# Optimization experiments

Measured on AMD Instinct MI355X. Metric: run time of the kernel, lower is better.

The kernel has to match this reference:

```python
import jax, jax.numpy as jnp
import numpy as np

B, Q, N, D = 16, 64, 16384, 128


def setup_inputs() -> dict:
    key = jax.random.key(0)
    k1, k2, k3 = jax.random.split(key, 3)
    query_vector = jax.random.normal(k1, (B, Q, D), dtype=jnp.float32)
    m_A = jax.random.normal(k2, (B, N, D), dtype=jnp.float32)
    # valid node counts per batch element, in [N//2, N] so masks are non-degenerate
    node_nums = jax.random.randint(k3, (B,), N // 2, N + 1, dtype=jnp.int32)
    return {"query_vector": query_vector, "m_A": m_A, "node_nums": node_nums}


def reference(query_vector, m_A, node_nums):
    # GraphPF.forward with num_supporting_node = -1 (default path).
    # prob_logits: [B, Q, N]
    prob_logits = jnp.einsum("bqd,bnd->bqn", query_vector, m_A)
    neg = jnp.finfo(prob_logits.dtype).min
    # get_attention_mask: additive mask, 0 for valid nodes, finfo.min for padding
    valid = jnp.arange(m_A.shape[1])[None, :] < node_nums[:, None]  # [B, N]
    attention_mask = jnp.where(valid, 0.0, neg).astype(prob_logits.dtype)[:, None, :]
    masked_logits = prob_logits + attention_mask
    prob_soft = jax.nn.softmax(masked_logits, axis=-1)
    res_vector = jnp.einsum("bqn,bnd->bqd", prob_soft, m_A)
    return (res_vector, prob_soft, prob_logits)
```

## Files before the change

kernel.cpp:

```cpp
#include <hip/hip_runtime.h>
#include <math.h>

#define Bn 16
#define Qn 64
#define Nn 16384
#define Dn 128
#define NT 128
#define NTILES (Nn / NT)
#define NCHUNK 512
#define NCHUNKS (Nn / NCHUNK)

#define RES_ELEMS  (Bn * Qn * Dn)
#define SOFT_OFF   (RES_ELEMS)
#define LOG_OFF    (RES_ELEMS + Bn * Qn * Nn)

#define NEGF (-3.4e38f)

typedef __attribute__((ext_vector_type(8))) short short8;
typedef float f32x4 __attribute__((ext_vector_type(4)));

typedef union { unsigned int u[4]; short8 v; } pk8;

__device__ __forceinline__ unsigned short f2bf(float x) {
    unsigned int u = __float_as_uint(x);
    return (unsigned short)((u + 0x7FFF + ((u >> 16) & 1)) >> 16);
}
__device__ __forceinline__ float bf2f(unsigned short h) {
    return __uint_as_float(((unsigned int)h) << 16);
}

__global__ __launch_bounds__(256) void k_logits(
    const float* __restrict__ qv, const float* __restrict__ A,
    const int* __restrict__ nodeNum,
    float* __restrict__ logits,
    float* __restrict__ pmax, float* __restrict__ psum)
{
    const int b = blockIdx.y, tile = blockIdx.x;
    const int n0 = tile * NT;
    const int tid = threadIdx.x;
    const int lane = tid & 63, wave = tid >> 6;
    const int qd = lane >> 4, cc = lane & 15;

    __shared__ __align__(16) unsigned char smem[55296];
    unsigned short* QHI = (unsigned short*)smem;
    unsigned short* QLO = QHI + 64 * 72;
    unsigned short* AHI = QLO + 64 * 72;
    unsigned short* ALO = AHI + 128 * 72;
    float* CB   = (float*)smem;
    float* REDM = ((float*)smem) + 64 * 132;
    float* REDS = REDM + 64 * 17;

    f32x4 acc[4][2];
#pragma unroll
    for (int mi = 0; mi < 4; mi++)
#pragma unroll
        for (int ni = 0; ni < 2; ni++) acc[mi][ni] = 0.f;

    const float* qb = qv + (size_t)b * Qn * Dn;
    const float* Ab = A  + (size_t)b * Nn * Dn + (size_t)n0 * Dn;

    for (int kk = 0; kk < Dn; kk += 64) {
        __syncthreads();
#pragma unroll
        for (int t = 0; t < 4; t++) {
            int u = tid + t * 256;
            int row = u >> 4, c4 = u & 15;
            float4 v = *(const float4*)(qb + row * Dn + kk + c4 * 4);
            ushort4 hi, lo;
            hi.x = f2bf(v.x); lo.x = f2bf(v.x - bf2f(hi.x));
            hi.y = f2bf(v.y); lo.y = f2bf(v.y - bf2f(hi.y));
            hi.z = f2bf(v.z); lo.z = f2bf(v.z - bf2f(hi.z));
            hi.w = f2bf(v.w); lo.w = f2bf(v.w - bf2f(hi.w));
            *(ushort4*)(QHI + row * 72 + c4 * 4) = hi;
            *(ushort4*)(QLO + row * 72 + c4 * 4) = lo;
        }
#pragma unroll
        for (int t = 0; t < 8; t++) {
            int u = tid + t * 256;
            int row = u >> 4, c4 = u & 15;
            float4 v = *(const float4*)(Ab + row * Dn + kk + c4 * 4);
            ushort4 hi, lo;
            hi.x = f2bf(v.x); lo.x = f2bf(v.x - bf2f(hi.x));
            hi.y = f2bf(v.y); lo.y = f2bf(v.y - bf2f(hi.y));
            hi.z = f2bf(v.z); lo.z = f2bf(v.z - bf2f(hi.z));
            hi.w = f2bf(v.w); lo.w = f2bf(v.w - bf2f(hi.w));
            *(ushort4*)(AHI + row * 72 + c4 * 4) = hi;
            *(ushort4*)(ALO + row * 72 + c4 * 4) = lo;
        }
        __syncthreads();
#pragma unroll
        for (int ks = 0; ks < 64; ks += 32) {
            const int ko = ks + qd * 8;
            short8 qh[4], ql[4], ah[2], al[2];
#pragma unroll
            for (int mi = 0; mi < 4; mi++) {
                int r = mi * 16 + cc;
                qh[mi] = *(const short8*)(QHI + r * 72 + ko);
                ql[mi] = *(const short8*)(QLO + r * 72 + ko);
            }
#pragma unroll
            for (int ni = 0; ni < 2; ni++) {
                int r = (wave * 2 + ni) * 16 + cc;
                ah[ni] = *(const short8*)(AHI + r * 72 + ko);
                al[ni] = *(const short8*)(ALO + r * 72 + ko);
            }
#pragma unroll
            for (int mi = 0; mi < 4; mi++)
#pragma unroll
                for (int ni = 0; ni < 2; ni++) {
                    acc[mi][ni] = __builtin_amdgcn_mfma_f32_16x16x32_bf16(
                        ql[mi], ah[ni], acc[mi][ni], 0, 0, 0);
                    acc[mi][ni] = __builtin_amdgcn_mfma_f32_16x16x32_bf16(
                        qh[mi], al[ni], acc[mi][ni], 0, 0, 0);
                    acc[mi][ni] = __builtin_amdgcn_mfma_f32_16x16x32_bf16(
                        qh[mi], ah[ni], acc[mi][ni], 0, 0, 0);
                }
        }
    }

    __syncthreads();
#pragma unroll
    for (int mi = 0; mi < 4; mi++)
#pragma unroll
        for (int ni = 0; ni < 2; ni++)
#pragma unroll
            for (int r = 0; r < 4; r++) {
                int q = mi * 16 + qd * 4 + r;
                int n = (wave * 2 + ni) * 16 + cc;
                CB[q * 132 + n] = acc[mi][ni][r];
            }
    __syncthreads();

    const int nv = nodeNum[b];
#pragma unroll
    for (int t = 0; t < 8; t++) {
        int u = tid + t * 256;
        int q = u >> 5, ng = u & 31;
        float4 v = *(const float4*)(CB + q * 132 + ng * 4);
        *(float4*)(logits + ((size_t)(b * Qn + q)) * Nn + n0 + ng * 4) = v;
    }
#pragma unroll
    for (int t = 0; t < 4; t++) {
        int u = tid + t * 256;
        int q = u >> 4, c = u & 15;
        const float* base = CB + q * 132 + c * 8;
        float m = NEGF;
#pragma unroll
        for (int j = 0; j < 8; j++)
            if (n0 + c * 8 + j < nv) m = fmaxf(m, base[j]);
        float s = 0.f;
#pragma unroll
        for (int j = 0; j < 8; j++)
            if (n0 + c * 8 + j < nv) s += __expf(base[j] - m);
        REDM[q * 17 + c] = m;
        REDS[q * 17 + c] = s;
    }
    __syncthreads();
    if (tid < Qn) {
        int q = tid;
        float M = NEGF;
#pragma unroll
        for (int t = 0; t < 16; t++) M = fmaxf(M, REDM[q * 17 + t]);
        float S = 0.f;
#pragma unroll
        for (int t = 0; t < 16; t++)
            S += REDS[q * 17 + t] * __expf(REDM[q * 17 + t] - M);
        pmax[((size_t)(b * Qn + q)) * NTILES + tile] = M;
        psum[((size_t)(b * Qn + q)) * NTILES + tile] = S;
    }
}

__global__ __launch_bounds__(64) void k_rows(
    const float* __restrict__ pmax, const float* __restrict__ psum,
    float* __restrict__ Mrow, float* __restrict__ invL)
{
    const int row = blockIdx.x;
    const int t = threadIdx.x;
    const float* pm = pmax + (size_t)row * NTILES;
    const float* ps = psum + (size_t)row * NTILES;
    float m0 = pm[t], m1 = pm[t + 64];
    float s0 = ps[t], s1 = ps[t + 64];
    float m = fmaxf(m0, m1);
#pragma unroll
    for (int o = 32; o >= 1; o >>= 1) m = fmaxf(m, __shfl_xor(m, o, 64));
    float s = s0 * __expf(m0 - m) + s1 * __expf(m1 - m);
#pragma unroll
    for (int o = 32; o >= 1; o >>= 1) s += __shfl_xor(s, o, 64);
    if (t == 0) { Mrow[row] = m; invL[row] = 1.0f / s; }
}

__global__ __launch_bounds__(256) void k_pv(
    const float* __restrict__ A, const int* __restrict__ nodeNum,
    const float* __restrict__ logits,
    const float* __restrict__ Mrow, const float* __restrict__ invL,
    float* __restrict__ soft, float* __restrict__ partial)
{
    const int b = blockIdx.y, chunk = blockIdx.x;
    const int tid = threadIdx.x;
    const int lane = tid & 63, wave = tid >> 6;
    const int qd = lane >> 4, cc = lane & 15;

    __shared__ __align__(16) unsigned short PS[64 * 40];
    __shared__ __align__(16) unsigned int  TMP2[16 * 132];
    __shared__ float MS[64], LS[64];

    if (tid < Qn) {
        MS[tid] = Mrow[b * Qn + tid];
        LS[tid] = invL[b * Qn + tid];
    }

    f32x4 acc[4][2];
#pragma unroll
    for (int mi = 0; mi < 4; mi++)
#pragma unroll
        for (int ni = 0; ni < 2; ni++) acc[mi][ni] = 0.f;

    const int nv = nodeNum[b];
    const float* Abase = A + (size_t)b * Nn * Dn;

    for (int s = 0; s < 16; s++) {
        const int n0 = chunk * NCHUNK + s * 32;
        __syncthreads();

#pragma unroll
        for (int t = 0; t < 2; t++) {
            int u = tid + t * 256;
            int q = u >> 3, ng = u & 7;
            size_t go = ((size_t)(b * Qn + q)) * Nn + n0 + ng * 4;
            float4 l4 = *(const float4*)(logits + go);
            float mq = MS[q], iq = LS[q];
            int nb = n0 + ng * 4;
            float4 p;
            p.x = (nb + 0 < nv) ? __expf(l4.x - mq) * iq : 0.f;
            p.y = (nb + 1 < nv) ? __expf(l4.y - mq) * iq : 0.f;
            p.z = (nb + 2 < nv) ? __expf(l4.z - mq) * iq : 0.f;
            p.w = (nb + 3 < nv) ? __expf(l4.w - mq) * iq : 0.f;
            *(float4*)(soft + go) = p;
            unsigned int d0 = (unsigned)f2bf(p.x) | ((unsigned)f2bf(p.y) << 16);
            unsigned int d1 = (unsigned)f2bf(p.z) | ((unsigned)f2bf(p.w) << 16);
            unsigned int* dst = (unsigned int*)(PS + q * 40 + ng * 4);
            dst[0] = d0; dst[1] = d1;
        }
#pragma unroll
        for (int t = 0; t < 2; t++) {
            int u = tid + t * 256;
            int n2 = u >> 5, db = u & 31;
            const float* r0 = Abase + (size_t)(n0 + n2 * 2) * Dn + db * 4;
            float4 a0 = *(const float4*)r0;
            float4 a1 = *(const float4*)(r0 + Dn);
            uint4 w;
            w.x = (unsigned)f2bf(a0.x) | ((unsigned)f2bf(a1.x) << 16);
            w.y = (unsigned)f2bf(a0.y) | ((unsigned)f2bf(a1.y) << 16);
            w.z = (unsigned)f2bf(a0.z) | ((unsigned)f2bf(a1.z) << 16);
            w.w = (unsigned)f2bf(a0.w) | ((unsigned)f2bf(a1.w) << 16);
            *(uint4*)(TMP2 + n2 * 132 + db * 4) = w;
        }
        __syncthreads();

        short8 pf[4];
#pragma unroll
        for (int mi = 0; mi < 4; mi++)
            pf[mi] = *(const short8*)(PS + (mi * 16 + cc) * 40 + qd * 8);
#pragma unroll
        for (int ni = 0; ni < 2; ni++) {
            int d = (wave * 2 + ni) * 16 + cc;
            pk8 bfr;
#pragma unroll
            for (int j = 0; j < 4; j++)
                bfr.u[j] = TMP2[(qd * 4 + j) * 132 + d];
#pragma unroll
            for (int mi = 0; mi < 4; mi++)
                acc[mi][ni] = __builtin_amdgcn_mfma_f32_16x16x32_bf16(
                    pf[mi], bfr.v, acc[mi][ni], 0, 0, 0);
        }
    }

    float* pout = partial + (size_t)chunk * RES_ELEMS + (size_t)(b * Qn) * Dn;
#pragma unroll
    for (int mi = 0; mi < 4; mi++)
#pragma unroll
        for (int ni = 0; ni < 2; ni++)
#pragma unroll
            for (int r = 0; r < 4; r++) {
                int q = mi * 16 + qd * 4 + r;
                int d = (wave * 2 + ni) * 16 + cc;
                pout[q * Dn + d] = acc[mi][ni][r];
            }
}

__global__ __launch_bounds__(256) void k_red(
    const float* __restrict__ partial, float* __restrict__ res)
{
    int g = blockIdx.x * 256 + threadIdx.x;
    float s = 0.f;
#pragma unroll
    for (int t = 0; t < NCHUNKS; t++)
        s += partial[(size_t)t * RES_ELEMS + g];
    res[g] = s;
}

extern "C" void kernel_launch(void* const* d_in, const int* in_sizes, int n_in,
                              void* d_out, int out_size, void* d_ws, size_t ws_size,
                              hipStream_t stream) {
    const float* qv = (const float*)d_in[0];
    const float* A  = (const float*)d_in[1];
    const int*   nn = (const int*)d_in[2];

    float* out    = (float*)d_out;
    float* res    = out;
    float* soft   = out + SOFT_OFF;
    float* logits = out + LOG_OFF;

    float* ws      = (float*)d_ws;
    float* pmax    = ws;
    float* psum    = pmax + (size_t)Bn * Qn * NTILES;
    float* Mrow    = psum + (size_t)Bn * Qn * NTILES;
    float* invL    = Mrow + Bn * Qn;
    float* partial = invL + Bn * Qn;

    dim3 blk(256);
    k_logits<<<dim3(NTILES, Bn), blk, 0, stream>>>(qv, A, nn, logits, pmax, psum);
    k_rows<<<Bn * Qn, 64, 0, stream>>>(pmax, psum, Mrow, invL);
    k_pv<<<dim3(NCHUNKS, Bn), blk, 0, stream>>>(A, nn, logits, Mrow, invL, soft, partial);
    k_red<<<RES_ELEMS / 256, blk, 0, stream>>>(partial, res);
}
```

Measured before the change: 295.5 us.

## Use packed bf16 conversion, swizzled LDS, atomic output reduction, smaller PV chunks

Replaces software bf16 rounding with the packed hardware convert instruction, and switches the logits kernel's padded LDS layout to an XOR swizzle so it uses less shared memory. It also adds occupancy hints to both GEMM kernels. The PV stage now uses half-size chunks, giving twice as many blocks, and accumulates into the result with atomic adds instead of writing partials and running a separate reduction kernel. A small zeroing kernel is added. Atomics make the summation order nondeterministic and add contention on the output.

```diff
diff --git a/kernel.cpp b/kernel.cpp
--- a/kernel.cpp
+++ b/kernel.cpp
@@ -7,7 +7,7 @@
 #define Dn 128
 #define NT 128
 #define NTILES (Nn / NT)
-#define NCHUNK 512
+#define NCHUNK 256
 #define NCHUNKS (Nn / NCHUNK)
 
 #define RES_ELEMS  (Bn * Qn * Dn)
@@ -21,15 +21,24 @@
 
 typedef union { unsigned int u[4]; short8 v; } pk8;
 
-__device__ __forceinline__ unsigned short f2bf(float x) {
-    unsigned int u = __float_as_uint(x);
-    return (unsigned short)((u + 0x7FFF + ((u >> 16) & 1)) >> 16);
-}
-__device__ __forceinline__ float bf2f(unsigned short h) {
-    return __uint_as_float(((unsigned int)h) << 16);
-}
-
-__global__ __launch_bounds__(256) void k_logits(
+__device__ __forceinline__ unsigned int cvt_pk_bf16(float a, float b) {
+    unsigned int r;
+    asm("v_cvt_pk_bf16_f32 %0, %1, %2" : "=v"(r) : "v"(a), "v"(b));
+    return r;
+}
+
+__device__ __forceinline__ int swz(int row, int col) {
+    return row * 64 + (col ^ ((row & 7) << 3));
+}
+
+__global__ __launch_bounds__(256) void k_zero(float* __restrict__ res)
+{
+    int g = blockIdx.x * 256 + threadIdx.x;
+    float4 z; z.x = 0.f; z.y = 0.f; z.z = 0.f; z.w = 0.f;
+    ((float4*)res)[g] = z;
+}
+
+__global__ __launch_bounds__(256, 3) void k_logits(
     const float* __restrict__ qv, const float* __restrict__ A,
     const int* __restrict__ nodeNum,
     float* __restrict__ logits,
@@ -41,11 +50,11 @@
     const int lane = tid & 63, wave = tid >> 6;
     const int qd = lane >> 4, cc = lane & 15;
 
-    __shared__ __align__(16) unsigned char smem[55296];
+    __shared__ __align__(16) unsigned char smem[49152];
     unsigned short* QHI = (unsigned short*)smem;
-    unsigned short* QLO = QHI + 64 * 72;
-    unsigned short* AHI = QLO + 64 * 72;
-    unsigned short* ALO = AHI + 128 * 72;
+    unsigned short* QLO = QHI + 64 * 64;
+    unsigned short* AHI = QLO + 64 * 64;
+    unsigned short* ALO = AHI + 128 * 64;
     float* CB   = (float*)smem;
     float* REDM = ((float*)smem) + 64 * 132;
     float* REDS = REDM + 64 * 17;
@@ -59,33 +68,45 @@
     const float* qb = qv + (size_t)b * Qn * Dn;
     const float* Ab = A  + (size_t)b * Nn * Dn + (size_t)n0 * Dn;
 
+    const int r16 = tid >> 4, c4 = tid & 15;
+
     for (int kk = 0; kk < Dn; kk += 64) {
         __syncthreads();
 #pragma unroll
         for (int t = 0; t < 4; t++) {
-            int u = tid + t * 256;
-            int row = u >> 4, c4 = u & 15;
-            float4 v = *(const float4*)(qb + row * Dn + kk + c4 * 4);
-            ushort4 hi, lo;
-            hi.x = f2bf(v.x); lo.x = f2bf(v.x - bf2f(hi.x));
-            hi.y = f2bf(v.y); lo.y = f2bf(v.y - bf2f(hi.y));
-            hi.z = f2bf(v.z); lo.z = f2bf(v.z - bf2f(hi.z));
-            hi.w = f2bf(v.w); lo.w = f2bf(v.w - bf2f(hi.w));
-            *(ushort4*)(QHI + row * 72 + c4 * 4) = hi;
-            *(ushort4*)(QLO + row * 72 + c4 * 4) = lo;
+            int row = r16 + 16 * t;
+            float4 v = *(const float4*)(qb + (size_t)row * Dn + kk + c4 * 4);
+            unsigned int h01 = cvt_pk_bf16(v.x, v.y);
+            unsigned int h23 = cvt_pk_bf16(v.z, v.w);
+            float rx = v.x - __uint_as_float(h01 << 16);
+            float ry = v.y - __uint_as_float(h01 & 0xFFFF0000u);
+            float rz = v.z - __uint_as_float(h23 << 16);
+            float rw = v.w - __uint_as_float(h23 & 0xFFFF0000u);
+            unsigned int l01 = cvt_pk_bf16(rx, ry);
+            unsigned int l23 = cvt_pk_bf16(rz, rw);
+            int idx = swz(row, c4 * 4);
+            uint2 hh; hh.x = h01; hh.y = h23;
+            uint2 ll; ll.x = l01; ll.y = l23;
+            *(uint2*)(QHI + idx) = hh;
+            *(uint2*)(QLO + idx) = ll;
         }
 #pragma unroll
         for (int t = 0; t < 8; t++) {
-            int u = tid + t * 256;
-            int row = u >> 4, c4 = u & 15;
-            float4 v = *(const float4*)(Ab + row * Dn + kk + c4 * 4);
-            ushort4 hi, lo;
-            hi.x = f2bf(v.x); lo.x = f2bf(v.x - bf2f(hi.x));
-            hi.y = f2bf(v.y); lo.y = f2bf(v.y - bf2f(hi.y));
-            hi.z = f2bf(v.z); lo.z = f2bf(v.z - bf2f(hi.z));
-            hi.w = f2bf(v.w); lo.w = f2bf(v.w - bf2f(hi.w));
-            *(ushort4*)(AHI + row * 72 + c4 * 4) = hi;
-            *(ushort4*)(ALO + row * 72 + c4 * 4) = lo;
+            int row = r16 + 16 * t;
+            float4 v = *(const float4*)(Ab + (size_t)row * Dn + kk + c4 * 4);
+            unsigned int h01 = cvt_pk_bf16(v.x, v.y);
+            unsigned int h23 = cvt_pk_bf16(v.z, v.w);
+            float rx = v.x - __uint_as_float(h01 << 16);
+            float ry = v.y - __uint_as_float(h01 & 0xFFFF0000u);
+            float rz = v.z - __uint_as_float(h23 << 16);
+            float rw = v.w - __uint_as_float(h23 & 0xFFFF0000u);
+            unsigned int l01 = cvt_pk_bf16(rx, ry);
+            unsigned int l23 = cvt_pk_bf16(rz, rw);
+            int idx = swz(row, c4 * 4);
+            uint2 hh; hh.x = h01; hh.y = h23;
+            uint2 ll; ll.x = l01; ll.y = l23;
+            *(uint2*)(AHI + idx) = hh;
+            *(uint2*)(ALO + idx) = ll;
         }
         __syncthreads();
 #pragma unroll
@@ -95,14 +116,16 @@
 #pragma unroll
             for (int mi = 0; mi < 4; mi++) {
                 int r = mi * 16 + cc;
-                qh[mi] = *(const short8*)(QHI + r * 72 + ko);
-                ql[mi] = *(const short8*)(QLO + r * 72 + ko);
+                int idx = swz(r, ko);
+                qh[mi] = *(const short8*)(QHI + idx);
+                ql[mi] = *(const short8*)(QLO + idx);
             }
 #pragma unroll
             for (int ni = 0; ni < 2; ni++) {
                 int r = (wave * 2 + ni) * 16 + cc;
-                ah[ni] = *(const short8*)(AHI + r * 72 + ko);
-                al[ni] = *(const short8*)(ALO + r * 72 + ko);
+                int idx = swz(r, ko);
+                ah[ni] = *(const short8*)(AHI + idx);
+                al[ni] = *(const short8*)(ALO + idx);
             }
 #pragma unroll
             for (int mi = 0; mi < 4; mi++)
@@ -189,11 +212,11 @@
     if (t == 0) { Mrow[row] = m; invL[row] = 1.0f / s; }
 }
 
-__global__ __launch_bounds__(256) void k_pv(
+__global__ __launch_bounds__(256, 4) void k_pv(
     const float* __restrict__ A, const int* __restrict__ nodeNum,
     const float* __restrict__ logits,
     const float* __restrict__ Mrow, const float* __restrict__ invL,
-    float* __restrict__ soft, float* __restrict__ partial)
+    float* __restrict__ soft, float* __restrict__ res)
 {
     const int b = blockIdx.y, chunk = blockIdx.x;
     const int tid = threadIdx.x;
@@ -218,7 +241,7 @@
     const int nv = nodeNum[b];
     const float* Abase = A + (size_t)b * Nn * Dn;
 
-    for (int s = 0; s < 16; s++) {
+    for (int s = 0; s < NCHUNK / 32; s++) {
         const int n0 = chunk * NCHUNK + s * 32;
         __syncthreads();
 
@@ -236,10 +259,9 @@
             p.z = (nb + 2 < nv) ? __expf(l4.z - mq) * iq : 0.f;
             p.w = (nb + 3 < nv) ? __expf(l4.w - mq) * iq : 0.f;
             *(float4*)(soft + go) = p;
-            unsigned int d0 = (unsigned)f2bf(p.x) | ((unsigned)f2bf(p.y) << 16);
-            unsigned int d1 = (unsigned)f2bf(p.z) | ((unsigned)f2bf(p.w) << 16);
             unsigned int* dst = (unsigned int*)(PS + q * 40 + ng * 4);
-            dst[0] = d0; dst[1] = d1;
+            dst[0] = cvt_pk_bf16(p.x, p.y);
+            dst[1] = cvt_pk_bf16(p.z, p.w);
         }
 #pragma unroll
         for (int t = 0; t < 2; t++) {
@@ -249,10 +271,10 @@
             float4 a0 = *(const float4*)r0;
             float4 a1 = *(const float4*)(r0 + Dn);
             uint4 w;
-            w.x = (unsigned)f2bf(a0.x) | ((unsigned)f2bf(a1.x) << 16);
-            w.y = (unsigned)f2bf(a0.y) | ((unsigned)f2bf(a1.y) << 16);
-            w.z = (unsigned)f2bf(a0.z) | ((unsigned)f2bf(a1.z) << 16);
-            w.w = (unsigned)f2bf(a0.w) | ((unsigned)f2bf(a1.w) << 16);
+            w.x = cvt_pk_bf16(a0.x, a1.x);
+            w.y = cvt_pk_bf16(a0.y, a1.y);
+            w.z = cvt_pk_bf16(a0.z, a1.z);
+            w.w = cvt_pk_bf16(a0.w, a1.w);
             *(uint4*)(TMP2 + n2 * 132 + db * 4) = w;
         }
         __syncthreads();
@@ -275,7 +297,7 @@
         }
     }
 
-    float* pout = partial + (size_t)chunk * RES_ELEMS + (size_t)(b * Qn) * Dn;
+    float* pout = res + (size_t)(b * Qn) * Dn;
 #pragma unroll
     for (int mi = 0; mi < 4; mi++)
 #pragma unroll
@@ -284,19 +306,8 @@
             for (int r = 0; r < 4; r++) {
                 int q = mi * 16 + qd * 4 + r;
                 int d = (wave * 2 + ni) * 16 + cc;
-                pout[q * Dn + d] = acc[mi][ni][r];
+                atomicAdd(&pout[q * Dn + d], acc[mi][ni][r]);
             }
-}
-
-__global__ __launch_bounds__(256) void k_red(
-    const float* __restrict__ partial, float* __restrict__ res)
-{
-    int g = blockIdx.x * 256 + threadIdx.x;
-    float s = 0.f;
-#pragma unroll
-    for (int t = 0; t < NCHUNKS; t++)
-        s += partial[(size_t)t * RES_ELEMS + g];
-    res[g] = s;
 }
 
 extern "C" void kernel_launch(void* const* d_in, const int* in_sizes, int n_in,
@@ -316,11 +327,10 @@
     float* psum    = pmax + (size_t)Bn * Qn * NTILES;
     float* Mrow    = psum + (size_t)Bn * Qn * NTILES;
     float* invL    = Mrow + Bn * Qn;
-    float* partial = invL + Bn * Qn;
 
     dim3 blk(256);
+    k_zero<<<RES_ELEMS / 1024, blk, 0, stream>>>(res);
     k_logits<<<dim3(NTILES, Bn), blk, 0, stream>>>(qv, A, nn, logits, pmax, psum);
     k_rows<<<Bn * Qn, 64, 0, stream>>>(pmax, psum, Mrow, invL);
-    k_pv<<<dim3(NCHUNKS, Bn), blk, 0, stream>>>(A, nn, logits, Mrow, invL, soft, partial);
-    k_red<<<RES_ELEMS / 256, blk, 0, stream>>>(partial, res);
-}
+    k_pv<<<dim3(NCHUNKS, Bn), blk, 0, stream>>>(A, nn, logits, Mrow, invL, soft, res);
+}
```

After: 290.0 us. About the same (-1.9%).
